# Kernel tuning notes

Measured on AMD Instinct MI355X. Metric: run time of the kernel, lower is better.

## Reference

```python
import jax, jax.numpy as jnp
import numpy as np

N = 50000      # nodes
E = 500000     # edges (before self-loops)
IN = 128       # input_channels
HID = 64       # hidden_channels
HEADS = 4
OUT = 10       # output_channels
G = 64         # number of graphs in batch


def setup_inputs() -> dict:
    key = jax.random.key(0)
    ks = jax.random.split(key, 12)
    x = jax.random.normal(ks[0], (N, IN), jnp.float32)
    edge_index = jax.random.randint(ks[1], (2, E), 0, N, jnp.int32)
    edge_weight = jax.random.uniform(ks[2], (E,), jnp.float32)
    batch = jnp.sort(jax.random.randint(ks[3], (N,), 0, G, jnp.int32))
    # GATConv layer 1: heads=4, concat=True
    W1 = jax.random.normal(ks[4], (HEADS * HID, IN), jnp.float32) / np.sqrt(IN)
    att_src1 = jax.random.normal(ks[5], (1, HEADS, HID), jnp.float32) / np.sqrt(HID)
    att_dst1 = jax.random.normal(ks[6], (1, HEADS, HID), jnp.float32) / np.sqrt(HID)
    b1 = jnp.zeros((HEADS * HID,), jnp.float32)
    # GATConv layer 2: heads=1, concat=False
    W2 = jax.random.normal(ks[7], (OUT, HEADS * HID), jnp.float32) / np.sqrt(HEADS * HID)
    att_src2 = jax.random.normal(ks[8], (1, 1, OUT), jnp.float32) / np.sqrt(OUT)
    att_dst2 = jax.random.normal(ks[9], (1, 1, OUT), jnp.float32) / np.sqrt(OUT)
    b2 = jnp.zeros((OUT,), jnp.float32)
    return {"x": x, "edge_index": edge_index, "edge_weight": edge_weight, "batch": batch,
            "W1": W1, "att_src1": att_src1, "att_dst1": att_dst1, "b1": b1,
            "W2": W2, "att_src2": att_src2, "att_dst2": att_dst2, "b2": b2}


def _gat_layer(x, src, dst, W, a_src, a_dst, heads, ch, n):
    # x: [n, in] -> h: [n, heads, ch]
    h = (x @ W.T).reshape(n, heads, ch)
    alpha_s = (h * a_src).sum(-1)  # [n, heads]
    alpha_d = (h * a_dst).sum(-1)
    e = jax.nn.leaky_relu(alpha_s[src] + alpha_d[dst], 0.2)  # [E', heads]
    # segment softmax over incoming edges of each destination node
    emax = jax.ops.segment_max(e, dst, num_segments=n)
    emax = jnp.where(jnp.isfinite(emax), emax, 0.0)
    ee = jnp.exp(e - emax[dst])
    denom = jax.ops.segment_sum(ee, dst, num_segments=n)
    alpha = ee / (denom[dst] + 1e-16)
    # weighted scatter-add of source features
    return jax.ops.segment_sum(alpha[:, :, None] * h[src], dst, num_segments=n)


def reference(x, edge_index, edge_weight, batch, W1, att_src1, att_dst1, b1,
              W2, att_src2, att_dst2, b2):
    # eval mode: dropout inactive; edge_weight is ignored by GATConv (as in source)
    n = x.shape[0]
    loops = jnp.arange(n, dtype=edge_index.dtype)  # PyG add_self_loops=True
    src = jnp.concatenate([edge_index[0], loops])
    dst = jnp.concatenate([edge_index[1], loops])
    h1 = _gat_layer(x, src, dst, W1, att_src1, att_dst1, HEADS, HID, n)
    h1 = jax.nn.elu(h1.reshape(n, HEADS * HID) + b1)
    h2 = _gat_layer(h1, src, dst, W2, att_src2, att_dst2, 1, OUT, n)[:, 0, :] + b2
    # global mean pool over graphs
    counts = jax.ops.segment_sum(jnp.ones((n,), h2.dtype), batch, num_segments=G)
    pooled = jax.ops.segment_sum(h2, batch, num_segments=G) / jnp.maximum(counts, 1.0)[:, None]
    return jax.nn.log_softmax(pooled, axis=1)
```

## Files before the change

### kernel.cpp

```cpp
#include <hip/hip_runtime.h>
#include <hip/hip_bf16.h>
#include <math.h>

#define NN 50000
#define EE 500000
#define ETOT (EE + NN)
#define NG 64

typedef __attribute__((ext_vector_type(8))) short short8v;
typedef __attribute__((ext_vector_type(4))) float float4v;
typedef __attribute__((ext_vector_type(2))) float float2v;

__device__ __forceinline__ float bf2f(unsigned short u) {
    unsigned int v = ((unsigned int)u) << 16;
    return __builtin_bit_cast(float, v);
}
__device__ __forceinline__ unsigned short f2bf(float f) {
    __hip_bfloat16 h = __float2bfloat16(f);
    return *(unsigned short*)&h;
}
__device__ __forceinline__ unsigned char f2fp8_hw(float f) {
    return (unsigned char)(__builtin_amdgcn_cvt_pk_fp8_f32(f, f, 0, false) & 0xff);
}

__global__ void k_setup(uint4* __restrict__ zp, int n16, int zB,
                        const float* __restrict__ W1, unsigned short* __restrict__ wb,
                        const float* __restrict__ x, unsigned short* __restrict__ xb) {
    int b = blockIdx.x;
    if (b < zB) {
        int t = b * 256 + threadIdx.x;
        if (t < n16) zp[t] = make_uint4(0, 0, 0, 0);
    } else if (b < zB + 128) {
        int t = (b - zB) * 256 + threadIdx.x;
        wb[t] = f2bf(W1[t]);
    } else {
        int t = (b - zB - 128) * 256 + threadIdx.x;
        if (t < NN * 128 / 8) {
            float4 a = *(const float4*)&x[(size_t)t * 8];
            float4 c = *(const float4*)&x[(size_t)t * 8 + 4];
            float f[8] = {a.x, a.y, a.z, a.w, c.x, c.y, c.z, c.w};
            short8v vh;
#pragma unroll
            for (int j = 0; j < 8; ++j) vh[j] = (short)f2bf(f[j]);
            *(short8v*)&xb[(size_t)t * 8] = vh;
        }
    }
}

__global__ void k_hist(const int* __restrict__ ei, const int* __restrict__ batch,
                       int* __restrict__ counts, int* __restrict__ ord,
                       int* __restrict__ gcount) {
    int t = blockIdx.x * 256 + threadIdx.x;
    if (t < ETOT) {
        int dst = (t < EE) ? ei[EE + t] : (t - EE);
        ord[t] = atomicAdd(counts + dst, 1);
    }
    if (t < NN) {
        int g = batch[t];
        int g0 = __shfl(g, 0);
        bool same = (g == g0);
        unsigned long long m = __ballot(same);
        if (same) {
            if ((threadIdx.x & 63) == (__ffsll((long long)m) - 1))
                atomicAdd(gcount + g0, (int)__popcll(m));
        } else {
            atomicAdd(gcount + g, 1);
        }
    }
}

__global__ void k_scan(const int* __restrict__ counts, int* __restrict__ indptr) {
    __shared__ int wsum[16];
    __shared__ int carry_s;
    int tid = threadIdx.x;
    int lane = tid & 63;
    int w = tid >> 6;
    int4 v[13];
#pragma unroll
    for (int c = 0; c < 13; ++c) {
        int i = c * 4096 + tid * 4;
        if (i + 3 < NN) {
            v[c] = *(const int4*)&counts[i];
        } else {
            v[c] = make_int4(0, 0, 0, 0);
            if (i < NN) v[c].x = counts[i];
            if (i + 1 < NN) v[c].y = counts[i + 1];
            if (i + 2 < NN) v[c].z = counts[i + 2];
        }
    }
    if (tid == 0) carry_s = 0;
    __syncthreads();
#pragma unroll
    for (int c = 0; c < 13; ++c) {
        int i = c * 4096 + tid * 4;
        int v0 = v[c].x, v1 = v[c].y, v2 = v[c].z, v3 = v[c].w;
        int tot = v0 + v1 + v2 + v3;
        int s = tot;
#pragma unroll
        for (int off = 1; off < 64; off <<= 1) {
            int u = __shfl_up(s, off);
            if (lane >= off) s += u;
        }
        if (lane == 63) wsum[w] = s;
        __syncthreads();
        if (w == 0) {
            int t2 = (lane < 16) ? wsum[lane] : 0;
#pragma unroll
            for (int off = 1; off < 16; off <<= 1) {
                int u = __shfl_up(t2, off);
                if (lane >= off) t2 += u;
            }
            if (lane < 16) wsum[lane] = t2;
        }
        __syncthreads();
        int wpre = (w == 0) ? 0 : wsum[w - 1];
        int incl = s + wpre;
        int carry = carry_s;
        int e = carry + incl - tot;
        if (i < NN)     indptr[i] = e;
        if (i + 1 < NN) indptr[i + 1] = e + v0;
        if (i + 2 < NN) indptr[i + 2] = e + v0 + v1;
        if (i + 3 < NN) indptr[i + 3] = e + v0 + v1 + v2;
        __syncthreads();
        if (tid == 1023) carry_s = carry + incl;
        __syncthreads();
    }
    if (tid == 0) indptr[NN] = carry_s;
}

__global__ __launch_bounds__(256) void k_gemm1(const unsigned short* __restrict__ xb,
                                               const unsigned short* __restrict__ wb,
                                               const float* __restrict__ att_s,
                                               const float* __restrict__ att_d,
                                               unsigned char* __restrict__ h1f8,
                                               float* __restrict__ alpha_s,
                                               float* __restrict__ alpha_d) {
    int w = threadIdx.x >> 6;
    int l = threadIdx.x & 63;
    int bm0 = blockIdx.x * 32;
    int i16 = l & 15;
    int kb = (l >> 4) * 8;
    int colb = w * 64;

    short8v a[2][4];
#pragma unroll
    for (int mi = 0; mi < 2; ++mi) {
        int r = bm0 + mi * 16 + i16;
#pragma unroll
        for (int k = 0; k < 4; ++k) {
            if (r < NN) a[mi][k] = *(const short8v*)&xb[(size_t)r * 128 + k * 32 + kb];
            else        a[mi][k] = (short8v){0,0,0,0,0,0,0,0};
        }
    }

    float4v acc[2][4];
#pragma unroll
    for (int mi = 0; mi < 2; ++mi)
#pragma unroll
        for (int ni = 0; ni < 4; ++ni)
            acc[mi][ni] = (float4v){0.f, 0.f, 0.f, 0.f};

#pragma unroll
    for (int k = 0; k < 4; ++k) {
#pragma unroll
        for (int ni = 0; ni < 4; ++ni) {
            short8v b = *(const short8v*)&wb[(size_t)(colb + ni * 16 + i16) * 128 + k * 32 + kb];
            acc[0][ni] = __builtin_amdgcn_mfma_f32_16x16x32_bf16(a[0][k], b, acc[0][ni], 0, 0, 0);
            acc[1][ni] = __builtin_amdgcn_mfma_f32_16x16x32_bf16(a[1][k], b, acc[1][ni], 0, 0, 0);
        }
    }

    int drb = (l >> 4) * 4;
    int dc = l & 15;
    float asw[4], adw[4];
#pragma unroll
    for (int ni = 0; ni < 4; ++ni) {
        asw[ni] = att_s[colb + ni * 16 + dc];
        adw[ni] = att_d[colb + ni * 16 + dc];
    }
#pragma unroll
    for (int mi = 0; mi < 2; ++mi) {
#pragma unroll
        for (int r = 0; r < 4; ++r) {
            int row = bm0 + mi * 16 + drb + r;
            float s = 0.f, d = 0.f;
#pragma unroll
            for (int ni = 0; ni < 4; ++ni) {
                float v = acc[mi][ni][r];
                s += v * asw[ni];
                d += v * adw[ni];
                if (row < NN)
                    h1f8[(size_t)row * 256 + colb + ni * 16 + dc] = f2fp8_hw(v);
            }
#pragma unroll
            for (int m = 8; m >= 1; m >>= 1) {
                s += __shfl_xor(s, m);
                d += __shfl_xor(d, m);
            }
            if (dc == 0 && row < NN) {
                alpha_s[row * 4 + w] = s;
                alpha_d[row * 4 + w] = d;
            }
        }
    }
}

__global__ void k_fill(const int* __restrict__ ei, const int* __restrict__ indptr,
                       const int* __restrict__ ord,
                       const float* __restrict__ als, const float* __restrict__ ald,
                       uint4* __restrict__ edges) {
    int t = blockIdx.x * 256 + threadIdx.x;
    if (t >= ETOT) return;
    int src = (t < EE) ? ei[t] : (t - EE);
    int dst = (t < EE) ? ei[EE + t] : (t - EE);
    int p = indptr[dst] + ord[t];
    float4 as = *(const float4*)&als[src * 4];
    float4 ad = *(const float4*)&ald[dst * 4];
    float e0 = as.x + ad.x, e1 = as.y + ad.y, e2 = as.z + ad.z, e3 = as.w + ad.w;
    e0 = e0 > 0.f ? e0 : 0.2f * e0;
    e1 = e1 > 0.f ? e1 : 0.2f * e1;
    e2 = e2 > 0.f ? e2 : 0.2f * e2;
    e3 = e3 > 0.f ? e3 : 0.2f * e3;
    unsigned int ee01 = (unsigned int)f2bf(__expf(e0)) | ((unsigned int)f2bf(__expf(e1)) << 16);
    unsigned int ee23 = (unsigned int)f2bf(__expf(e2)) | ((unsigned int)f2bf(__expf(e3)) << 16);
    edges[p] = make_uint4((unsigned int)src, ee01, ee23, (unsigned int)dst);
}

__global__ void k_gather1(const int* __restrict__ indptr, const uint4* __restrict__ edges,
                          const unsigned char* __restrict__ h1f8, const float* __restrict__ b1,
                          const float* __restrict__ W2, const float* __restrict__ as2v,
                          const float* __restrict__ ad2v, float* __restrict__ h2lin,
                          float* __restrict__ als2, float* __restrict__ ald2) {
    int wid = (blockIdx.x * 256 + threadIdx.x) >> 6;
    int l = threadIdx.x & 63;
    if (wid >= NN) return;
    int p0 = __builtin_amdgcn_readfirstlane(indptr[wid]);
    int p1 = __builtin_amdgcn_readfirstlane(indptr[wid + 1]);
    int head = l >> 4;
    int hsh = (head & 1) * 16;
    float acc0 = 0.f, acc1 = 0.f, acc2 = 0.f, acc3 = 0.f, dsum = 0.f;
    int p = p0;
    for (; p + 7 < p1; p += 8) {
        uint4 e[8];
#pragma unroll
        for (int j = 0; j < 8; ++j) e[j] = edges[p + j];
        unsigned int hv[8];
#pragma unroll
        for (int j = 0; j < 8; ++j)
            hv[j] = *(const unsigned int*)&h1f8[(size_t)e[j].x * 256 + l * 4];
#pragma unroll
        for (int j = 0; j < 8; ++j) {
            unsigned int packed = (head & 2) ? e[j].z : e[j].y;
            float wgt = bf2f((unsigned short)(packed >> hsh));
            float2v lo = __builtin_amdgcn_cvt_pk_f32_fp8(hv[j], false);
            float2v hi = __builtin_amdgcn_cvt_pk_f32_fp8(hv[j], true);
            dsum += wgt;
            acc0 += wgt * lo.x;
            acc1 += wgt * lo.y;
            acc2 += wgt * hi.x;
            acc3 += wgt * hi.y;
        }
    }
    for (; p < p1; ++p) {
        uint4 e = edges[p];
        unsigned int hv = *(const unsigned int*)&h1f8[(size_t)e.x * 256 + l * 4];
        unsigned int packed = (head & 2) ? e.z : e.y;
        float wgt = bf2f((unsigned short)(packed >> hsh));
        float2v lo = __builtin_amdgcn_cvt_pk_f32_fp8(hv, false);
        float2v hi = __builtin_amdgcn_cvt_pk_f32_fp8(hv, true);
        dsum += wgt;
        acc0 += wgt * lo.x;
        acc1 += wgt * lo.y;
        acc2 += wgt * hi.x;
        acc3 += wgt * hi.y;
    }
    float inv = 1.0f / dsum;
    float4 bv = *(const float4*)&b1[l * 4];
    float o0 = acc0 * inv + bv.x;
    float o1 = acc1 * inv + bv.y;
    float o2 = acc2 * inv + bv.z;
    float o3 = acc3 * inv + bv.w;
    o0 = o0 > 0.f ? o0 : expm1f(o0);
    o1 = o1 > 0.f ? o1 : expm1f(o1);
    o2 = o2 > 0.f ? o2 : expm1f(o2);
    o3 = o3 > 0.f ? o3 : expm1f(o3);
    float t[10];
#pragma unroll
    for (int o = 0; o < 10; ++o) {
        float4 wv = *(const float4*)&W2[o * 256 + l * 4];
        t[o] = o0 * wv.x + o1 * wv.y + o2 * wv.z + o3 * wv.w;
    }
#pragma unroll
    for (int m = 32; m > 0; m >>= 1) {
#pragma unroll
        for (int o = 0; o < 10; ++o) t[o] += __shfl_xor(t[o], m);
    }
    if (l == 0) {
        float as = 0.f, ad = 0.f;
#pragma unroll
        for (int o = 0; o < 10; ++o) {
            h2lin[(size_t)wid * 16 + o] = t[o];
            as += t[o] * as2v[o];
            ad += t[o] * ad2v[o];
        }
        als2[wid] = as;
        ald2[wid] = ad;
    }
}

__global__ void k_g2pool(const int* __restrict__ indptr, const uint4* __restrict__ edges,
                         const float* __restrict__ als2, const float* __restrict__ ald2,
                         const float* __restrict__ h2lin, const float* __restrict__ b2,
                         const int* __restrict__ batch, float* __restrict__ pooled) {
    int wave = (blockIdx.x * 256 + threadIdx.x) >> 6;
    int lane = threadIdx.x & 63;
    int grp = lane >> 4, c = lane & 15;
    int node = wave * 4 + grp;
    float acc = 0.f;
    int g = -1;
    if (node < NN) {
        int p0 = indptr[node], p1 = indptr[node + 1];
        float ad2n = ald2[node];
        float dsum = 0.f;
        int p = p0;
        for (; p + 3 < p1; p += 4) {
            uint4 e0 = edges[p], e1 = edges[p + 1], e2 = edges[p + 2], e3 = edges[p + 3];
            float v0 = als2[e0.x] + ad2n;
            float v1 = als2[e1.x] + ad2n;
            float v2 = als2[e2.x] + ad2n;
            float v3 = als2[e3.x] + ad2n;
            float h0 = 0.f, h1_ = 0.f, h2 = 0.f, h3 = 0.f;
            if (c < 10) {
                h0 = h2lin[(size_t)e0.x * 16 + c];
                h1_ = h2lin[(size_t)e1.x * 16 + c];
                h2 = h2lin[(size_t)e2.x * 16 + c];
                h3 = h2lin[(size_t)e3.x * 16 + c];
            }
            v0 = v0 > 0.f ? v0 : 0.2f * v0;
            v1 = v1 > 0.f ? v1 : 0.2f * v1;
            v2 = v2 > 0.f ? v2 : 0.2f * v2;
            v3 = v3 > 0.f ? v3 : 0.2f * v3;
            float w0 = __expf(v0), w1 = __expf(v1), w2 = __expf(v2), w3 = __expf(v3);
            dsum += (w0 + w1) + (w2 + w3);
            acc += w0 * h0 + w1 * h1_ + w2 * h2 + w3 * h3;
        }
        for (; p < p1; ++p) {
            uint4 e = edges[p];
            float v = als2[e.x] + ad2n;
            v = v > 0.f ? v : 0.2f * v;
            float w = __expf(v);
            dsum += w;
            if (c < 10) acc += w * h2lin[(size_t)e.x * 16 + c];
        }
        if (c < 10) acc = acc / dsum + b2[c];
        else acc = 0.f;
        g = batch[node];
    }
    int g0 = __shfl(g, 0);
    bool uni = __all((node >= NN) || (g == g0));
    if (uni) {
        if (g0 >= 0) {
            acc += __shfl_xor(acc, 16);
            acc += __shfl_xor(acc, 32);
            if (grp == 0 && c < 10)
                atomicAdd(pooled + g0 * 10 + c, acc);
        }
    } else if (node < NN && c < 10) {
        atomicAdd(pooled + g * 10 + c, acc);
    }
}

__global__ void k_final(const float* __restrict__ pooled, const int* __restrict__ gcount,
                        float* __restrict__ out) {
    int g = threadIdx.x;
    if (g >= NG) return;
    float c = fmaxf((float)gcount[g], 1.0f);
    float m[10];
    float mx = -1e30f;
#pragma unroll
    for (int i = 0; i < 10; ++i) {
        m[i] = pooled[g * 10 + i] / c;
        mx = fmaxf(mx, m[i]);
    }
    float s = 0.f;
#pragma unroll
    for (int i = 0; i < 10; ++i) s += expf(m[i] - mx);
    float lse = mx + logf(s);
#pragma unroll
    for (int i = 0; i < 10; ++i) out[g * 10 + i] = m[i] - lse;
}

extern "C" void kernel_launch(void* const* d_in, const int* in_sizes, int n_in,
                              void* d_out, int out_size, void* d_ws, size_t ws_size,
                              hipStream_t stream) {
    const float* x   = (const float*)d_in[0];
    const int*   ei  = (const int*)d_in[1];
    const int*   bat = (const int*)d_in[3];
    const float* W1  = (const float*)d_in[4];
    const float* as1 = (const float*)d_in[5];
    const float* ad1 = (const float*)d_in[6];
    const float* b1  = (const float*)d_in[7];
    const float* W2  = (const float*)d_in[8];
    const float* as2 = (const float*)d_in[9];
    const float* ad2 = (const float*)d_in[10];
    const float* b2  = (const float*)d_in[11];
    float* out = (float*)d_out;

    char* ws = (char*)d_ws;
    size_t off = 0;
    auto alloc = [&](size_t bytes) -> size_t {
        size_t o = off;
        off = (off + bytes + 255) & ~(size_t)255;
        return o;
    };
    size_t o_counts = alloc((size_t)NN * 4);
    size_t o_pooled = alloc((size_t)NG * 10 * 4);
    size_t o_gcount = alloc((size_t)NG * 4);
    size_t zero_bytes = off;
    size_t o_ord    = alloc((size_t)ETOT * 4);
    size_t o_indptr = alloc((size_t)(NN + 1) * 4);
    size_t o_edges  = alloc((size_t)ETOT * 16);
    size_t o_h1f8   = alloc((size_t)NN * 256);
    size_t o_als1   = alloc((size_t)NN * 4 * 4);
    size_t o_ald1   = alloc((size_t)NN * 4 * 4);
    size_t o_h2lin  = alloc((size_t)NN * 16 * 4);
    size_t o_als2   = alloc((size_t)NN * 4);
    size_t o_ald2   = alloc((size_t)NN * 4);
    size_t o_wb     = alloc((size_t)256 * 128 * 2);
    size_t o_xb     = alloc((size_t)NN * 128 * 2);
    (void)ws_size;

    int*   counts = (int*)(ws + o_counts);
    float* pooled = (float*)(ws + o_pooled);
    int*   gcount = (int*)(ws + o_gcount);
    int*   ord    = (int*)(ws + o_ord);
    int*   indptr = (int*)(ws + o_indptr);
    uint4* edges  = (uint4*)(ws + o_edges);
    unsigned char*  h1f8 = (unsigned char*)(ws + o_h1f8);
    float* als1   = (float*)(ws + o_als1);
    float* ald1   = (float*)(ws + o_ald1);
    float* h2lin  = (float*)(ws + o_h2lin);
    float* als2   = (float*)(ws + o_als2);
    float* ald2   = (float*)(ws + o_ald2);
    unsigned short* wb = (unsigned short*)(ws + o_wb);
    unsigned short* xb = (unsigned short*)(ws + o_xb);

    int n16 = (int)(zero_bytes / 16);
    int zB = (n16 + 255) / 256;
    int xB = (NN * 128 / 8 + 255) / 256;
    int gE = (ETOT + 255) / 256;
    int gW = (NN + 3) / 4;

    k_setup<<<zB + 128 + xB, 256, 0, stream>>>((uint4*)ws, n16, zB, W1, wb, x, xb);
    k_hist<<<gE, 256, 0, stream>>>(ei, bat, counts, ord, gcount);
    k_scan<<<1, 1024, 0, stream>>>(counts, indptr);
    k_gemm1<<<(NN + 31) / 32, 256, 0, stream>>>(xb, wb, as1, ad1, h1f8, als1, ald1);
    k_fill<<<gE, 256, 0, stream>>>(ei, indptr, ord, als1, ald1, edges);
    k_gather1<<<gW, 256, 0, stream>>>(indptr, edges, h1f8, b1, W2, as2, ad2,
                                      h2lin, als2, ald2);
    k_g2pool<<<gW, 256, 0, stream>>>(indptr, edges, als2, ald2, h2lin, b2, bat, pooled);
    k_final<<<1, 64, 0, stream>>>(pooled, gcount, out);
    (void)n_in; (void)in_sizes; (void)out_size;
}
```

Before: 176.1 us.

## Pack fp8 h1 stores into dwords and predicate gather remainder loops

The GEMM epilogue now converts four accumulator values into one packed fp8 dword and writes it with a single 32-bit store, replacing four byte stores. This reorders the h1 column layout, so the gather kernel remaps its bias and W2 indices to the interleaved columns. Both gather kernels drop their scalar tail loops: loads past the end are clamped to the last edge and their weights are zeroed, so every edge runs through the unrolled batch. The cost is some redundant loads and wasted lanes on nodes with few edges.

```diff
diff --git a/kernel.cpp b/kernel.cpp
--- a/kernel.cpp
+++ b/kernel.cpp
@@ -18,9 +18,6 @@
 __device__ __forceinline__ unsigned short f2bf(float f) {
     __hip_bfloat16 h = __float2bfloat16(f);
     return *(unsigned short*)&h;
-}
-__device__ __forceinline__ unsigned char f2fp8_hw(float f) {
-    return (unsigned char)(__builtin_amdgcn_cvt_pk_fp8_f32(f, f, 0, false) & 0xff);
 }
 
 __global__ void k_setup(uint4* __restrict__ zp, int n16, int zB,
@@ -183,15 +180,14 @@
 #pragma unroll
         for (int r = 0; r < 4; ++r) {
             int row = bm0 + mi * 16 + drb + r;
-            float s = 0.f, d = 0.f;
-#pragma unroll
-            for (int ni = 0; ni < 4; ++ni) {
-                float v = acc[mi][ni][r];
-                s += v * asw[ni];
-                d += v * adw[ni];
-                if (row < NN)
-                    h1f8[(size_t)row * 256 + colb + ni * 16 + dc] = f2fp8_hw(v);
-            }
+            float v0 = acc[mi][0][r], v1 = acc[mi][1][r];
+            float v2 = acc[mi][2][r], v3 = acc[mi][3][r];
+            float s = v0 * asw[0] + v1 * asw[1] + v2 * asw[2] + v3 * asw[3];
+            float d = v0 * adw[0] + v1 * adw[1] + v2 * adw[2] + v3 * adw[3];
+            unsigned int packed = __builtin_amdgcn_cvt_pk_fp8_f32(v0, v1, 0u, false);
+            packed = __builtin_amdgcn_cvt_pk_fp8_f32(v2, v3, packed, true);
+            if (row < NN)
+                *(unsigned int*)&h1f8[(size_t)row * 256 + colb + dc * 4] = packed;
 #pragma unroll
             for (int m = 8; m >= 1; m >>= 1) {
                 s += __shfl_xor(s, m);
@@ -236,22 +232,27 @@
     if (wid >= NN) return;
     int p0 = __builtin_amdgcn_readfirstlane(indptr[wid]);
     int p1 = __builtin_amdgcn_readfirstlane(indptr[wid + 1]);
+    int last = p1 - 1;
     int head = l >> 4;
     int hsh = (head & 1) * 16;
+    const unsigned char* hb = h1f8 + l * 4;
     float acc0 = 0.f, acc1 = 0.f, acc2 = 0.f, acc3 = 0.f, dsum = 0.f;
-    int p = p0;
-    for (; p + 7 < p1; p += 8) {
+    for (int p = p0; p < p1; p += 8) {
         uint4 e[8];
 #pragma unroll
-        for (int j = 0; j < 8; ++j) e[j] = edges[p + j];
+        for (int j = 0; j < 8; ++j) {
+            int idx = p + j;
+            e[j] = edges[idx < p1 ? idx : last];
+        }
         unsigned int hv[8];
 #pragma unroll
         for (int j = 0; j < 8; ++j)
-            hv[j] = *(const unsigned int*)&h1f8[(size_t)e[j].x * 256 + l * 4];
+            hv[j] = *(const unsigned int*)(hb + (size_t)e[j].x * 256);
 #pragma unroll
         for (int j = 0; j < 8; ++j) {
             unsigned int packed = (head & 2) ? e[j].z : e[j].y;
             float wgt = bf2f((unsigned short)(packed >> hsh));
+            wgt = (p + j < p1) ? wgt : 0.f;
             float2v lo = __builtin_amdgcn_cvt_pk_f32_fp8(hv[j], false);
             float2v hi = __builtin_amdgcn_cvt_pk_f32_fp8(hv[j], true);
             dsum += wgt;
@@ -261,25 +262,12 @@
             acc3 += wgt * hi.y;
         }
     }
-    for (; p < p1; ++p) {
-        uint4 e = edges[p];
-        unsigned int hv = *(const unsigned int*)&h1f8[(size_t)e.x * 256 + l * 4];
-        unsigned int packed = (head & 2) ? e.z : e.y;
-        float wgt = bf2f((unsigned short)(packed >> hsh));
-        float2v lo = __builtin_amdgcn_cvt_pk_f32_fp8(hv, false);
-        float2v hi = __builtin_amdgcn_cvt_pk_f32_fp8(hv, true);
-        dsum += wgt;
-        acc0 += wgt * lo.x;
-        acc1 += wgt * lo.y;
-        acc2 += wgt * hi.x;
-        acc3 += wgt * hi.y;
-    }
     float inv = 1.0f / dsum;
-    float4 bv = *(const float4*)&b1[l * 4];
-    float o0 = acc0 * inv + bv.x;
-    float o1 = acc1 * inv + bv.y;
-    float o2 = acc2 * inv + bv.z;
-    float o3 = acc3 * inv + bv.w;
+    int cbase = head * 64 + (l & 15);
+    float o0 = acc0 * inv + b1[cbase];
+    float o1 = acc1 * inv + b1[cbase + 16];
+    float o2 = acc2 * inv + b1[cbase + 32];
+    float o3 = acc3 * inv + b1[cbase + 48];
     o0 = o0 > 0.f ? o0 : expm1f(o0);
     o1 = o1 > 0.f ? o1 : expm1f(o1);
     o2 = o2 > 0.f ? o2 : expm1f(o2);
@@ -287,8 +275,8 @@
     float t[10];
 #pragma unroll
     for (int o = 0; o < 10; ++o) {
-        float4 wv = *(const float4*)&W2[o * 256 + l * 4];
-        t[o] = o0 * wv.x + o1 * wv.y + o2 * wv.z + o3 * wv.w;
+        const float* wr = &W2[o * 256 + cbase];
+        t[o] = o0 * wr[0] + o1 * wr[16] + o2 * wr[32] + o3 * wr[48];
     }
 #pragma unroll
     for (int m = 32; m > 0; m >>= 1) {
@@ -320,11 +308,15 @@
     int g = -1;
     if (node < NN) {
         int p0 = indptr[node], p1 = indptr[node + 1];
+        int last = p1 - 1;
         float ad2n = ald2[node];
         float dsum = 0.f;
-        int p = p0;
-        for (; p + 3 < p1; p += 4) {
-            uint4 e0 = edges[p], e1 = edges[p + 1], e2 = edges[p + 2], e3 = edges[p + 3];
+        for (int p = p0; p < p1; p += 4) {
+            int i0 = p, i1 = p + 1, i2 = p + 2, i3 = p + 3;
+            uint4 e0 = edges[i0];
+            uint4 e1 = edges[i1 < p1 ? i1 : last];
+            uint4 e2 = edges[i2 < p1 ? i2 : last];
+            uint4 e3 = edges[i3 < p1 ? i3 : last];
             float v0 = als2[e0.x] + ad2n;
             float v1 = als2[e1.x] + ad2n;
             float v2 = als2[e2.x] + ad2n;
@@ -340,17 +332,12 @@
             v1 = v1 > 0.f ? v1 : 0.2f * v1;
             v2 = v2 > 0.f ? v2 : 0.2f * v2;
             v3 = v3 > 0.f ? v3 : 0.2f * v3;
-            float w0 = __expf(v0), w1 = __expf(v1), w2 = __expf(v2), w3 = __expf(v3);
+            float w0 = __expf(v0);
+            float w1 = (i1 < p1) ? __expf(v1) : 0.f;
+            float w2 = (i2 < p1) ? __expf(v2) : 0.f;
+            float w3 = (i3 < p1) ? __expf(v3) : 0.f;
             dsum += (w0 + w1) + (w2 + w3);
             acc += w0 * h0 + w1 * h1_ + w2 * h2 + w3 * h3;
-        }
-        for (; p < p1; ++p) {
-            uint4 e = edges[p];
-            float v = als2[e.x] + ad2n;
-            v = v > 0.f ? v : 0.2f * v;
-            float w = __expf(v);
-            dsum += w;
-            if (c < 10) acc += w * h2lin[(size_t)e.x * 16 + c];
         }
         if (c < 10) acc = acc / dsum + b2[c];
         else acc = 0.f;
```

Result: no change. 173.0 us (median of 2 runs) (-1.8%).
